# Performance work log

Hardware: AMD Instinct MI355X
Metric: run time of the kernel (lower is better)

The kernel has to match this reference:

```python
import jax, jax.numpy as jnp
import numpy as np

# Multi-scale AvgPool3d pyramid (stride 1, zero padding, count_include_pad=True as in torch)
KERNELS = [(1, 1, 1), (1, 5, 5), (3, 13, 13), (5, 23, 23), (7, 31, 31), (9, 41, 41)]
WEIGHTS = [w / 100.0 for w in [20, 20, 20, 20, 20, 20, 10, 10]]
EPS = 1e-7  # BatchDiceLoss epsilon


def avgpool3d(x, k):
    # x: [B, C, D, H, W]; separable sum-pool per axis then divide by full kernel size
    # (equivalent to torch AvgPool3d with count_include_pad=True, stride 1, pad=(k-1)//2)
    y = x
    for axis, ks in zip((2, 3, 4), k):
        if ks > 1:
            window = [1] * 5
            window[axis] = ks
            pad = [(0, 0)] * 5
            pad[axis] = (ks // 2, ks // 2)
            y = jax.lax.reduce_window(y, 0.0, jax.lax.add, tuple(window), (1,) * 5, tuple(pad))
    return y / float(np.prod(k))


def batch_dice(pred, target):
    # BatchDiceLoss([1.0]): single label channel 0, flattened over the whole batch
    p = pred[:, 0].reshape(-1)
    t = target[:, 0].reshape(-1)
    inter = jnp.sum(p * t)
    return 1.0 - (2.0 * inter) / (jnp.sum(p) + jnp.sum(t) + EPS)


def multi_scale_dc(pred, target):
    loss = 0.0
    for k in KERNELS:
        pp = avgpool3d(avgpool3d(pred, k), k)   # pool applied twice per scale
        tt = avgpool3d(avgpool3d(target, k), k)
        loss = loss + batch_dice(pp, tt)
    return loss / len(KERNELS)


def setup_inputs() -> dict:
    key = jax.random.key(0)
    ks = jax.random.split(key, 14)
    vol = (4, 1, 28, 160, 160)
    u = lambda k: jax.random.uniform(k, vol, dtype=jnp.float32)
    return {
        "pr_core_c": u(ks[0]),
        "pr_core_p": u(ks[1]),
        "gt_core": u(ks[2]),
        "pr_lesion_c": u(ks[3]),
        "pr_lesion_p": u(ks[4]),
        "gt_lesion": u(ks[5]),
        "pr_penu_c": u(ks[6]),
        "pr_penu_p": u(ks[7]),
        "gt_penu": u(ks[8]),
        "output": jax.random.uniform(ks[9], (4, 6, 28, 160, 160), dtype=jnp.float32),
        "off_core_c": jax.random.normal(ks[10], (4, 3), dtype=jnp.float32),
        "off_penu_p": jax.random.normal(ks[11], (4, 3), dtype=jnp.float32),
        "off_target_c": jax.random.normal(ks[12], (4, 3), dtype=jnp.float32),
        "off_target_p": jax.random.normal(ks[13], (4, 3), dtype=jnp.float32),
    }


def reference(pr_core_c, pr_core_p, gt_core, pr_lesion_c, pr_lesion_p, gt_lesion,
              pr_penu_c, pr_penu_p, gt_penu, output,
              off_core_c, off_penu_p, off_target_c, off_target_p):
    loss = WEIGHTS[0] * multi_scale_dc(pr_core_c, gt_core)
    loss += WEIGHTS[1] * multi_scale_dc(pr_core_p, gt_core)
    loss += WEIGHTS[2] * multi_scale_dc(pr_lesion_c, gt_lesion)
    loss += WEIGHTS[3] * multi_scale_dc(pr_lesion_p, gt_lesion)
    loss += WEIGHTS[4] * multi_scale_dc(pr_penu_c, gt_penu)
    loss += WEIGHTS[5] * multi_scale_dc(pr_penu_p, gt_penu)
    # temporal monotonicity penalty: mean(|diff| - diff) per consecutive time pair
    diff = output[:, 1:] - output[:, :-1]           # [B, T-1, D, H, W]
    loss += WEIGHTS[6] * jnp.sum(jnp.mean(jnp.abs(diff) - diff, axis=(0, 2, 3, 4)))
    loss += WEIGHTS[7] * jnp.mean(jnp.abs(off_core_c - off_target_c))
    loss += WEIGHTS[7] * jnp.mean(jnp.abs(off_penu_p - off_target_p))
    return loss
```

## Files before the change

### kernel.cpp

```cpp
#include <hip/hip_runtime.h>


#define DIMB 4
#define DIMD 28
#define DIMH 160
#define DIMW 160
#define HW   (DIMH * DIMW)
#define DHW  (DIMD * HW)
#define VOL_N (DIMB * DHW)
#define PGRID 640
#define NSLOTS 91
#define DICE_EPS 1e-7
#define TBL_OFF (480 * 1024)

__device__ __forceinline__ float u2f(int pos, int k, int L) {
    if (k == 1) return 1.f;
    int r = k >> 1;
    float s = 0.f;
    for (int j = max(pos - r, 0); j <= min(pos + r, L - 1); ++j)
        s += (float)(min(j + r, L - 1) - max(j - r, 0) + 1);
    return s / (float)(k * k);
}

__device__ __forceinline__ float wave_sum(float v) {
#pragma unroll
    for (int o = 1; o < 64; o <<= 1) v += __shfl_xor(v, o, 64);
    return v;
}

template<int K>
__device__ __forceinline__ void box4_col(float (&x)[28]) {
    constexpr int R = K / 2;
    constexpr float INVK = 1.f / (float)K;
#pragma unroll
    for (int p = 0; p < 4; ++p) {
        float y[28];
        float s = 0.f;
#pragma unroll
        for (int j = 0; j <= R; ++j) s += x[j];
        y[0] = s;
#pragma unroll
        for (int i = 1; i < 28; ++i) {
            if (i + R < 28) s += x[i + R];
            if (i - R - 1 >= 0) s -= x[i - R - 1];
            y[i] = s;
        }
#pragma unroll
        for (int i = 0; i < 28; ++i) x[i] = y[i] * INVK;
    }
}

template<int K>
__device__ __forceinline__ void hstore(const float (&raw)[40],
                                       unsigned char* __restrict__ ob,
                                       int l, int c, int wl, int h0)
{
    constexpr int R = K / 2;
    constexpr float INVK = 1.f / (float)K;
    float ox[40];
#pragma unroll
    for (int i = 0; i < 40; ++i) ox[i] = raw[i];
#pragma unroll
    for (int pass = 0; pass < 4; ++pass) {
        float lo[R], hi[R];
#pragma unroll
        for (int i = 0; i < R; ++i) {
            float a = __shfl(ox[40 - R + i], l - 16, 64);
            lo[i] = (c == 0) ? 0.f : a;
            float b = __shfl(ox[i], l + 16, 64);
            hi[i] = (c == 3) ? 0.f : b;
        }
#define HWIN(j) ((j) < R ? lo[(j)] : ((j) < R + 40 ? ox[(j) - R] : hi[(j) - R - 40]))
        float out[40];
        float s = 0.f;
#pragma unroll
        for (int j = 0; j <= 2 * R; ++j) s += HWIN(j);
        out[0] = s * INVK;
#pragma unroll
        for (int i = 1; i < 40; ++i) {
            s += HWIN(i + 2 * R) - HWIN(i - 1);
            out[i] = s * INVK;
        }
#undef HWIN
#pragma unroll
        for (int i = 0; i < 40; ++i) ox[i] = out[i];
    }
#pragma unroll
    for (int i = 0; i < 40; ++i)
        ob[(h0 + i) * DIMW + wl] = (unsigned char)__float2uint_rn(ox[i] * 255.f);
}

__global__ __launch_bounds__(256) void hpool_tbl(const float* __restrict__ g0,
    const float* __restrict__ g1, const float* __restrict__ g2,
    unsigned char* __restrict__ bufs, float* __restrict__ tbl)
{
    int bx = blockIdx.x;
    if (bx < 840) {
        int u = bx * 2 + (threadIdx.x >> 7);
        int tt = threadIdx.x & 127;
        int g = u / 560, r = u - g * 560;
        int bd = r / 5, wt = r - bd * 5;
        const float* in = (g == 0) ? g0 : (g == 1) ? g1 : g2;
        int l = tt & 63, v = tt >> 6;
        int c = l >> 4, wl = v * 16 + (l & 15), h0 = c * 40;
        const float* base = in + (size_t)bd * HW + wt * 32;
        float raw[40];
#pragma unroll
        for (int i = 0; i < 40; ++i) raw[i] = base[(h0 + i) * DIMW + wl];
        unsigned char* ob = bufs + (size_t)g * 5 * VOL_N + (size_t)bd * HW + wt * 32;
        hstore<5> (raw, ob + 0 * (size_t)VOL_N, l, c, wl, h0);
        hstore<13>(raw, ob + 1 * (size_t)VOL_N, l, c, wl, h0);
        hstore<23>(raw, ob + 2 * (size_t)VOL_N, l, c, wl, h0);
        hstore<31>(raw, ob + 3 * (size_t)VOL_N, l, c, wl, h0);
        hstore<41>(raw, ob + 4 * (size_t)VOL_N, l, c, wl, h0);
    } else {
        const int KDa[6] = {1, 1, 3, 5, 7, 9};
        const int KHa[6] = {1, 5, 13, 23, 31, 41};
        for (int e = threadIdx.x; e < 1128; e += 256) {
            if (e < 960) tbl[e] = u2f(e % 160, KHa[e / 160], DIMH);
            else {
                int q = e - 960;
                tbl[e] = u2f(q % 28, KDa[q / 28], DIMD);
            }
        }
    }
}

template<int K>
__device__ __forceinline__ void wpool_to_S(const unsigned char* __restrict__ tb,
    float (*S)[164], int t, int l, int rr, int c, bool act)
{
    constexpr int R = K / 2;
    const float INV = 1.0f / (255.0f * (float)K * (float)K * (float)K * (float)K);
    float ox[20];
#pragma unroll
    for (int i = 0; i < 20; ++i) ox[i] = 0.f;
    if (act) {
        unsigned int u[5];
#pragma unroll
        for (int q = 0; q < 5; ++q) u[q] = *(const unsigned int*)(tb + 4 * q);
#pragma unroll
        for (int q = 0; q < 5; ++q) {
#pragma unroll
            for (int j = 0; j < 4; ++j)
                ox[4 * q + j] = (float)((u[q] >> (8 * j)) & 0xFFu);
        }
    }
#pragma unroll
    for (int pass = 0; pass < 4; ++pass) {
        float lo[R], hi[R];
#pragma unroll
        for (int i = 0; i < R; ++i) {
            float a = __shfl(ox[20 - R + i], l - 1, 64);
            lo[i] = (c == 0) ? 0.f : a;
            float b = __shfl(ox[i], l + 1, 64);
            hi[i] = (c == 7) ? 0.f : b;
        }
#define WWIN(j) ((j) < R ? lo[(j)] : ((j) < R + 20 ? ox[(j) - R] : hi[(j) - R - 20]))
        float out[20];
        float s = 0.f;
#pragma unroll
        for (int j = 0; j <= 2 * R; ++j) s += WWIN(j);
        out[0] = s;
#pragma unroll
        for (int i = 1; i < 20; ++i) {
            s += WWIN(i + 2 * R) - WWIN(i - 1);
            out[i] = s;
        }
#undef WWIN
#pragma unroll
        for (int i = 0; i < 20; ++i) ox[i] = out[i];
    }
    if (act) {
#pragma unroll
        for (int i = 0; i < 20; ++i) S[rr][c * 20 + i] = ox[i] * INV;
    }
    __syncthreads();
}

template<int K, int KD>
__device__ __forceinline__ void wd_scale(const unsigned char* __restrict__ tb,
    const float4* __restrict__ c4, const float4* __restrict__ p4, int base4,
    float (*S)[164], float* red2, int t, int l, int wid, int rr, int c, bool act,
    double* __restrict__ partials, int slot_c, int slot_p, int bh)
{
    wpool_to_S<K>(tb, S, t, l, rr, c, act);
    if constexpr (KD > 1) {
        if (t < DIMW) {
            float col[28];
#pragma unroll
            for (int j = 0; j < 28; ++j) col[j] = S[j][t];
            box4_col<KD>(col);
#pragma unroll
            for (int j = 0; j < 28; ++j) S[j][t] = col[j];
        }
        __syncthreads();
    }
    float aic = 0.f, aip = 0.f;
    for (int e4 = t; e4 < 1120; e4 += 256) {
        int dd = e4 / 40, w4 = e4 - dd * 40;
        int fi = base4 + dd * (HW / 4) + w4;
        float4 vc = c4[fi], vp = p4[fi];
        const float4 sv = *(const float4*)&S[dd][4 * w4];
        aic += vc.x * sv.x + vc.y * sv.y + vc.z * sv.z + vc.w * sv.w;
        aip += vp.x * sv.x + vp.y * sv.y + vp.z * sv.z + vp.w * sv.w;
    }
    float r1 = wave_sum(aic), r2 = wave_sum(aip);
    if (l == 0) { red2[wid * 2] = r1; red2[wid * 2 + 1] = r2; }
    __syncthreads();
    if (t < 2) {
        double rv = (double)red2[t] + red2[2 + t] + red2[4 + t] + red2[6 + t];
        partials[(size_t)(t == 0 ? slot_c : slot_p) * PGRID + bh] = rv;
    }
}

__global__ __launch_bounds__(256) void wd_dot0(const unsigned char* __restrict__ bufs,
    const float* __restrict__ pc0, const float* __restrict__ pp0,
    const float* __restrict__ pc1, const float* __restrict__ pp1,
    const float* __restrict__ pc2, const float* __restrict__ pp2,
    const float* __restrict__ tr0, const float* __restrict__ tr1,
    const float* __restrict__ tr2, const float* __restrict__ o6,
    const float* __restrict__ tbl, double* __restrict__ partials)
{
    __shared__ __align__(16) float S[DIMD][164];
    __shared__ float redS[4][24];
    int bx0 = blockIdx.x;
    int t = threadIdx.x;

    if (bx0 < 640) {
        int mb = bx0;
        const int N4 = VOL_N / 4, PB = N4 / DIMB;
        float acc = 0.f;
        const float4* p = (const float4*)o6;
        for (int i = mb * 256 + t; i < N4; i += PGRID * 256) {
            int b = i / PB, r4 = i - b * PB;
            size_t a = (size_t)(b * 6) * PB + r4;
            float4 prev = p[a];
#pragma unroll
            for (int cc = 1; cc < 6; ++cc) {
                float4 cur = p[a + (size_t)cc * PB];
                acc += fmaxf(prev.x - cur.x, 0.f) + fmaxf(prev.y - cur.y, 0.f)
                     + fmaxf(prev.z - cur.z, 0.f) + fmaxf(prev.w - cur.w, 0.f);
                prev = cur;
            }
        }
        float rv = wave_sum(acc * 2.f);
        int lane = t & 63, wid = t >> 6;
        if (lane == 0) redS[wid][0] = rv;
        __syncthreads();
        if (t == 0)
            partials[(size_t)90 * PGRID + mb] =
                (double)redS[0][0] + redS[1][0] + redS[2][0] + redS[3][0];
        return;
    }

    int bxx = bx0 - 640;
    int w = (bxx & 7) * 1200 + (bxx >> 3);
    int u = w / 5, q = w - u * 5;
    int g = u / PGRID, bh = u - g * PGRID;
    int b = bh / DIMH, h = bh - b * DIMH;
    const float* pc = (g == 0) ? pc0 : (g == 1) ? pc1 : pc2;
    const float* pp = (g == 0) ? pp0 : (g == 1) ? pp1 : pp2;
    size_t base0 = (size_t)b * DHW + (size_t)h * DIMW;
    int base4 = b * (DHW / 4) + h * 40;
    const float4* c4 = (const float4*)pc;
    const float4* p4 = (const float4*)pp;
    int l = t & 63, wid = t >> 6;
    int rr = wid * 7 + (l >> 3), c = l & 7;
    bool act = (l < 56);
    int sbuf = (q < 4) ? (4 - q) : 0;
    const unsigned char* tb = bufs + (size_t)(g * 5 + sbuf) * VOL_N
                            + base0 + (size_t)rr * HW + c * 20;

    if (q < 4) {
        int s = 5 - q;
        int slot_c = (2 * g) * 6 + s, slot_p = (2 * g + 1) * 6 + s;
        switch (q) {
            case 0: wd_scale<41, 9>(tb, c4, p4, base4, S, &redS[0][0], t, l, wid, rr, c, act, partials, slot_c, slot_p, bh); break;
            case 1: wd_scale<31, 7>(tb, c4, p4, base4, S, &redS[0][0], t, l, wid, rr, c, act, partials, slot_c, slot_p, bh); break;
            case 2: wd_scale<23, 5>(tb, c4, p4, base4, S, &redS[0][0], t, l, wid, rr, c, act, partials, slot_c, slot_p, bh); break;
            default: wd_scale<13, 3>(tb, c4, p4, base4, S, &redS[0][0], t, l, wid, rr, c, act, partials, slot_c, slot_p, bh); break;
        }
        return;
    }

    const float* tr = (g == 0) ? tr0 : (g == 1) ? tr1 : tr2;
    const float4* t4 = (const float4*)tr;
    wpool_to_S<5>(tb, S, t, l, rr, c, act);
    float vals[22];
#pragma unroll
    for (int i = 0; i < 22; ++i) vals[i] = 0.f;
    for (int e4 = t; e4 < 1120; e4 += 256) {
        int dd = e4 / 40, w4 = e4 - dd * 40;
        int fi = base4 + dd * (HW / 4) + w4;
        float4 vc = c4[fi], vp = p4[fi], vt = t4[fi];
        const float4 sv = *(const float4*)&S[dd][4 * w4];
        vals[0] += vc.x*sv.x + vc.y*sv.y + vc.z*sv.z + vc.w*sv.w;
        vals[1] += vp.x*sv.x + vp.y*sv.y + vp.z*sv.z + vp.w*sv.w;
        vals[2] += vc.x*vt.x + vc.y*vt.y + vc.z*vt.z + vc.w*vt.w;
        vals[3] += vp.x*vt.x + vp.y*vt.y + vp.z*vt.z + vp.w*vt.w;
#pragma unroll
        for (int s = 0; s < 6; ++s) {
            float cdh = tbl[960 + s * 28 + dd];
            const float4 cw = *(const float4*)(tbl + s * 160 + 4 * w4);
            vals[4 + s]  += cdh * (cw.x*vc.x + cw.y*vc.y + cw.z*vc.z + cw.w*vc.w);
            vals[10 + s] += cdh * (cw.x*vp.x + cw.y*vp.y + cw.z*vp.z + cw.w*vp.w);
            vals[16 + s] += cdh * (cw.x*vt.x + cw.y*vt.y + cw.z*vt.z + cw.w*vt.w);
        }
    }
#pragma unroll
    for (int i = 0; i < 22; ++i) {
        float rv = wave_sum(vals[i]);
        if (l == 0) redS[wid][i] = rv;
    }
    __syncthreads();
    if (t < 22) {
        double rv = (double)redS[0][t] + redS[1][t] + redS[2][t] + redS[3][t];
        double fac = 1.0;
        int slot;
        if (t == 0) slot = (2 * g) * 6 + 1;
        else if (t == 1) slot = (2 * g + 1) * 6 + 1;
        else if (t == 2) slot = (2 * g) * 6;
        else if (t == 3) slot = (2 * g + 1) * 6;
        else {
            int i = t - 4, vv = i / 6, s = i % 6;
            fac = (double)tbl[s * 160 + h];
            slot = (vv == 0) ? 36 + (2 * g) * 6 + s
                 : (vv == 1) ? 36 + (2 * g + 1) * 6 + s
                             : 72 + g * 6 + s;
        }
        partials[(size_t)slot * PGRID + bh] = rv * fac;
    }
}

__global__ __launch_bounds__(64) void fin_pre(const double* __restrict__ partials,
                                              double* __restrict__ ssum)
{
    int slot = blockIdx.x, t = threadIdx.x;
    double a = 0.0;
    for (int i = t; i < PGRID; i += 64) a += partials[(size_t)slot * PGRID + i];
#pragma unroll
    for (int o = 1; o < 64; o <<= 1) a += __shfl_xor(a, o, 64);
    if (t == 0) ssum[slot] = a;
}

__global__ void finalize(const double* __restrict__ ssum,
                         const float* __restrict__ off_a,
                         const float* __restrict__ off_b,
                         const float* __restrict__ off_ta,
                         const float* __restrict__ off_tb,
                         float* __restrict__ out)
{
    if (threadIdx.x == 0) {
        double loss = 0.0;
        for (int pair = 0; pair < 6; ++pair) {
            for (int s = 0; s < 6; ++s) {
                double inter = ssum[pair * 6 + s];
                double sp = ssum[36 + pair * 6 + s];
                double st = ssum[72 + (pair / 2) * 6 + s];
                loss += 0.2 * (1.0 - 2.0 * inter / (sp + st + DICE_EPS)) / 6.0;
            }
        }
        loss += 0.1 * (ssum[90] / (double)VOL_N);
        double oa = 0.0, ob = 0.0;
        for (int i = 0; i < 12; ++i) {
            oa += fabs((double)off_a[i] - (double)off_ta[i]);
            ob += fabs((double)off_b[i] - (double)off_tb[i]);
        }
        loss += 0.1 * (oa / 12.0) + 0.1 * (ob / 12.0);
        out[0] = (float)loss;
    }
}

extern "C" void kernel_launch(void* const* d_in, const int* in_sizes, int n_in,
                              void* d_out, int out_size, void* d_ws, size_t ws_size,
                              hipStream_t stream)
{
    double* partials = (double*)d_ws;
    double* ssum = partials + (size_t)NSLOTS * PGRID;
    float* tbl = (float*)((char*)d_ws + TBL_OFF);
    unsigned char* bufs = (unsigned char*)d_ws + 512 * 1024;

    const float* pred[6] = {(const float*)d_in[0], (const float*)d_in[1],
                            (const float*)d_in[3], (const float*)d_in[4],
                            (const float*)d_in[6], (const float*)d_in[7]};
    const float* gt[3] = {(const float*)d_in[2], (const float*)d_in[5],
                          (const float*)d_in[8]};

    hpool_tbl<<<841, 256, 0, stream>>>(gt[0], gt[1], gt[2], bufs, tbl);
    wd_dot0<<<10240, 256, 0, stream>>>(bufs, pred[0], pred[1], pred[2], pred[3],
                                       pred[4], pred[5], gt[0], gt[1], gt[2],
                                       (const float*)d_in[9], tbl, partials);
    fin_pre<<<NSLOTS, 64, 0, stream>>>(partials, ssum);
    finalize<<<1, 64, 0, stream>>>(ssum,
                                   (const float*)d_in[10], (const float*)d_in[11],
                                   (const float*)d_in[12], (const float*)d_in[13],
                                   (float*)d_out);
}
```

Before: 135.7 us.

## Split scale-1 pool and dense dot blocks into separate uniform work groups

```diff
diff --git a/kernel.cpp b/kernel.cpp
--- a/kernel.cpp
+++ b/kernel.cpp
@@ -214,7 +214,7 @@
     }
 }
 
-__global__ __launch_bounds__(256) void wd_dot0(const unsigned char* __restrict__ bufs,
+__global__ __launch_bounds__(256) void wd_mix(const unsigned char* __restrict__ bufs,
     const float* __restrict__ pc0, const float* __restrict__ pp0,
     const float* __restrict__ pc1, const float* __restrict__ pp1,
     const float* __restrict__ pc2, const float* __restrict__ pp2,
@@ -227,110 +227,111 @@
     int bx0 = blockIdx.x;
     int t = threadIdx.x;
 
-    if (bx0 < 640) {
-        int mb = bx0;
-        const int N4 = VOL_N / 4, PB = N4 / DIMB;
-        float acc = 0.f;
-        const float4* p = (const float4*)o6;
-        for (int i = mb * 256 + t; i < N4; i += PGRID * 256) {
-            int b = i / PB, r4 = i - b * PB;
-            size_t a = (size_t)(b * 6) * PB + r4;
-            float4 prev = p[a];
-#pragma unroll
-            for (int cc = 1; cc < 6; ++cc) {
-                float4 cur = p[a + (size_t)cc * PB];
-                acc += fmaxf(prev.x - cur.x, 0.f) + fmaxf(prev.y - cur.y, 0.f)
-                     + fmaxf(prev.z - cur.z, 0.f) + fmaxf(prev.w - cur.w, 0.f);
-                prev = cur;
-            }
-        }
-        float rv = wave_sum(acc * 2.f);
-        int lane = t & 63, wid = t >> 6;
-        if (lane == 0) redS[wid][0] = rv;
-        __syncthreads();
-        if (t == 0)
-            partials[(size_t)90 * PGRID + mb] =
-                (double)redS[0][0] + redS[1][0] + redS[2][0] + redS[3][0];
-        return;
-    }
-
-    int bxx = bx0 - 640;
-    int w = (bxx & 7) * 1200 + (bxx >> 3);
-    int u = w / 5, q = w - u * 5;
-    int g = u / PGRID, bh = u - g * PGRID;
-    int b = bh / DIMH, h = bh - b * DIMH;
-    const float* pc = (g == 0) ? pc0 : (g == 1) ? pc1 : pc2;
-    const float* pp = (g == 0) ? pp0 : (g == 1) ? pp1 : pp2;
-    size_t base0 = (size_t)b * DHW + (size_t)h * DIMW;
-    int base4 = b * (DHW / 4) + h * 40;
-    const float4* c4 = (const float4*)pc;
-    const float4* p4 = (const float4*)pp;
-    int l = t & 63, wid = t >> 6;
-    int rr = wid * 7 + (l >> 3), c = l & 7;
-    bool act = (l < 56);
-    int sbuf = (q < 4) ? (4 - q) : 0;
-    const unsigned char* tb = bufs + (size_t)(g * 5 + sbuf) * VOL_N
-                            + base0 + (size_t)rr * HW + c * 20;
-
-    if (q < 4) {
+    if (bx0 < 9600) {
+        int w = (bx0 & 7) * 1200 + (bx0 >> 3);
+        int u = w / 5, q = w - u * 5;
+        int g = u / PGRID, bh = u - g * PGRID;
+        int b = bh / DIMH, h = bh - b * DIMH;
+        const float* pc = (g == 0) ? pc0 : (g == 1) ? pc1 : pc2;
+        const float* pp = (g == 0) ? pp0 : (g == 1) ? pp1 : pp2;
+        size_t base0 = (size_t)b * DHW + (size_t)h * DIMW;
+        int base4 = b * (DHW / 4) + h * 40;
+        const float4* c4 = (const float4*)pc;
+        const float4* p4 = (const float4*)pp;
+        int l = t & 63, wid = t >> 6;
+        int rr = wid * 7 + (l >> 3), c = l & 7;
+        bool act = (l < 56);
+        int sbuf = 4 - q;
+        const unsigned char* tb = bufs + (size_t)(g * 5 + sbuf) * VOL_N
+                                + base0 + (size_t)rr * HW + c * 20;
         int s = 5 - q;
         int slot_c = (2 * g) * 6 + s, slot_p = (2 * g + 1) * 6 + s;
         switch (q) {
             case 0: wd_scale<41, 9>(tb, c4, p4, base4, S, &redS[0][0], t, l, wid, rr, c, act, partials, slot_c, slot_p, bh); break;
             case 1: wd_scale<31, 7>(tb, c4, p4, base4, S, &redS[0][0], t, l, wid, rr, c, act, partials, slot_c, slot_p, bh); break;
             case 2: wd_scale<23, 5>(tb, c4, p4, base4, S, &redS[0][0], t, l, wid, rr, c, act, partials, slot_c, slot_p, bh); break;
-            default: wd_scale<13, 3>(tb, c4, p4, base4, S, &redS[0][0], t, l, wid, rr, c, act, partials, slot_c, slot_p, bh); break;
+            case 3: wd_scale<13, 3>(tb, c4, p4, base4, S, &redS[0][0], t, l, wid, rr, c, act, partials, slot_c, slot_p, bh); break;
+            default: wd_scale<5, 1>(tb, c4, p4, base4, S, &redS[0][0], t, l, wid, rr, c, act, partials, slot_c, slot_p, bh); break;
         }
         return;
     }
 
-    const float* tr = (g == 0) ? tr0 : (g == 1) ? tr1 : tr2;
-    const float4* t4 = (const float4*)tr;
-    wpool_to_S<5>(tb, S, t, l, rr, c, act);
-    float vals[22];
-#pragma unroll
-    for (int i = 0; i < 22; ++i) vals[i] = 0.f;
-    for (int e4 = t; e4 < 1120; e4 += 256) {
-        int dd = e4 / 40, w4 = e4 - dd * 40;
-        int fi = base4 + dd * (HW / 4) + w4;
-        float4 vc = c4[fi], vp = p4[fi], vt = t4[fi];
-        const float4 sv = *(const float4*)&S[dd][4 * w4];
-        vals[0] += vc.x*sv.x + vc.y*sv.y + vc.z*sv.z + vc.w*sv.w;
-        vals[1] += vp.x*sv.x + vp.y*sv.y + vp.z*sv.z + vp.w*sv.w;
-        vals[2] += vc.x*vt.x + vc.y*vt.y + vc.z*vt.z + vc.w*vt.w;
-        vals[3] += vp.x*vt.x + vp.y*vt.y + vp.z*vt.z + vp.w*vt.w;
-#pragma unroll
-        for (int s = 0; s < 6; ++s) {
-            float cdh = tbl[960 + s * 28 + dd];
-            const float4 cw = *(const float4*)(tbl + s * 160 + 4 * w4);
-            vals[4 + s]  += cdh * (cw.x*vc.x + cw.y*vc.y + cw.z*vc.z + cw.w*vc.w);
-            vals[10 + s] += cdh * (cw.x*vp.x + cw.y*vp.y + cw.z*vp.z + cw.w*vp.w);
-            vals[16 + s] += cdh * (cw.x*vt.x + cw.y*vt.y + cw.z*vt.z + cw.w*vt.w);
-        }
-    }
-#pragma unroll
-    for (int i = 0; i < 22; ++i) {
-        float rv = wave_sum(vals[i]);
-        if (l == 0) redS[wid][i] = rv;
-    }
+    if (bx0 < 11520) {
+        int db = bx0 - 9600;
+        int g = db / PGRID, blk = db - g * PGRID;
+        const float* pc = (g == 0) ? pc0 : (g == 1) ? pc1 : pc2;
+        const float* pp = (g == 0) ? pp0 : (g == 1) ? pp1 : pp2;
+        const float* tr = (g == 0) ? tr0 : (g == 1) ? tr1 : tr2;
+        const float4* c4p = (const float4*)pc;
+        const float4* p4p = (const float4*)pp;
+        const float4* t4p = (const float4*)tr;
+        float vals[20];
+#pragma unroll
+        for (int i = 0; i < 20; ++i) vals[i] = 0.f;
+        const int N4 = VOL_N / 4;
+        for (int i4 = blk * 256 + t; i4 < N4; i4 += PGRID * 256) {
+            int w4 = i4 % 40;
+            int rest = i4 / 40;
+            int h = rest % DIMH;
+            int d = (rest / DIMH) % DIMD;
+            float4 vc = c4p[i4], vp = p4p[i4], vt = t4p[i4];
+            vals[0] += vc.x*vt.x + vc.y*vt.y + vc.z*vt.z + vc.w*vt.w;
+            vals[1] += vp.x*vt.x + vp.y*vt.y + vp.z*vt.z + vp.w*vt.w;
+#pragma unroll
+            for (int s = 0; s < 6; ++s) {
+                float cdh = tbl[960 + s * 28 + d] * tbl[s * 160 + h];
+                const float4 cw = *(const float4*)(tbl + s * 160 + 4 * w4);
+                vals[2 + s]  += cdh * (cw.x*vc.x + cw.y*vc.y + cw.z*vc.z + cw.w*vc.w);
+                vals[8 + s]  += cdh * (cw.x*vp.x + cw.y*vp.y + cw.z*vp.z + cw.w*vp.w);
+                vals[14 + s] += cdh * (cw.x*vt.x + cw.y*vt.y + cw.z*vt.z + cw.w*vt.w);
+            }
+        }
+        int lane = t & 63, wid = t >> 6;
+#pragma unroll
+        for (int i = 0; i < 20; ++i) {
+            float rv = wave_sum(vals[i]);
+            if (lane == 0) redS[wid][i] = rv;
+        }
+        __syncthreads();
+        if (t < 20) {
+            double rv = (double)redS[0][t] + redS[1][t] + redS[2][t] + redS[3][t];
+            int slot;
+            if (t == 0) slot = (2 * g) * 6;
+            else if (t == 1) slot = (2 * g + 1) * 6;
+            else {
+                int i = t - 2, vv = i / 6, s = i % 6;
+                slot = (vv == 0) ? 36 + (2 * g) * 6 + s
+                     : (vv == 1) ? 36 + (2 * g + 1) * 6 + s
+                                 : 72 + g * 6 + s;
+            }
+            partials[(size_t)slot * PGRID + blk] = rv;
+        }
+        return;
+    }
+
+    int mb = bx0 - 11520;
+    const int N4 = VOL_N / 4, PB = N4 / DIMB;
+    float acc = 0.f;
+    const float4* p = (const float4*)o6;
+    for (int i = mb * 256 + t; i < N4; i += PGRID * 256) {
+        int b = i / PB, r4 = i - b * PB;
+        size_t a = (size_t)(b * 6) * PB + r4;
+        float4 prev = p[a];
+#pragma unroll
+        for (int cc = 1; cc < 6; ++cc) {
+            float4 cur = p[a + (size_t)cc * PB];
+            acc += fmaxf(prev.x - cur.x, 0.f) + fmaxf(prev.y - cur.y, 0.f)
+                 + fmaxf(prev.z - cur.z, 0.f) + fmaxf(prev.w - cur.w, 0.f);
+            prev = cur;
+        }
+    }
+    float rv = wave_sum(acc * 2.f);
+    int lane = t & 63, wid = t >> 6;
+    if (lane == 0) redS[wid][0] = rv;
     __syncthreads();
-    if (t < 22) {
-        double rv = (double)redS[0][t] + redS[1][t] + redS[2][t] + redS[3][t];
-        double fac = 1.0;
-        int slot;
-        if (t == 0) slot = (2 * g) * 6 + 1;
-        else if (t == 1) slot = (2 * g + 1) * 6 + 1;
-        else if (t == 2) slot = (2 * g) * 6;
-        else if (t == 3) slot = (2 * g + 1) * 6;
-        else {
-            int i = t - 4, vv = i / 6, s = i % 6;
-            fac = (double)tbl[s * 160 + h];
-            slot = (vv == 0) ? 36 + (2 * g) * 6 + s
-                 : (vv == 1) ? 36 + (2 * g + 1) * 6 + s
-                             : 72 + g * 6 + s;
-        }
-        partials[(size_t)slot * PGRID + bh] = rv * fac;
-    }
+    if (t == 0)
+        partials[(size_t)90 * PGRID + mb] =
+            (double)redS[0][0] + redS[1][0] + redS[2][0] + redS[3][0];
 }
 
 __global__ __launch_bounds__(64) void fin_pre(const double* __restrict__ partials,
@@ -388,9 +389,9 @@
                           (const float*)d_in[8]};
 
     hpool_tbl<<<841, 256, 0, stream>>>(gt[0], gt[1], gt[2], bufs, tbl);
-    wd_dot0<<<10240, 256, 0, stream>>>(bufs, pred[0], pred[1], pred[2], pred[3],
-                                       pred[4], pred[5], gt[0], gt[1], gt[2],
-                                       (const float*)d_in[9], tbl, partials);
+    wd_mix<<<12160, 256, 0, stream>>>(bufs, pred[0], pred[1], pred[2], pred[3],
+                                      pred[4], pred[5], gt[0], gt[1], gt[2],
+                                      (const float*)d_in[9], tbl, partials);
     fin_pre<<<NSLOTS, 64, 0, stream>>>(partials, ssum);
     finalize<<<1, 64, 0, stream>>>(ssum,
                                    (const float*)d_in[10], (const float*)d_in[11],
```

Result: no change. 133.3 us (-1.8%).
